# Kernel tuning notes

Measured on AMD Instinct MI355X. Metric: run time of the kernel, lower is better.

## Reference

```python
import jax, jax.numpy as jnp
import numpy as np

B, T, HID, NH = 2, 2048, 1024, 16
HD = HID // NH  # head_dim = 64
ROPE_BASE = 1000000.0


def _precompute_freqs(dim, end, rope_base):
    inv = 1.0 / (rope_base ** (np.arange(0, dim, 2)[: dim // 2].astype(np.float32) / dim))
    t = np.arange(end, dtype=np.float32)
    freqs = np.outer(t, inv).astype(np.float32)  # (end, dim//2)
    cos = np.concatenate([np.cos(freqs), np.cos(freqs)], axis=-1)
    sin = np.concatenate([np.sin(freqs), np.sin(freqs)], axis=-1)
    return jnp.asarray(cos), jnp.asarray(sin)


def setup_inputs() -> dict:
    key = jax.random.key(0)
    ks = jax.random.split(key, 5)
    x = jax.random.normal(ks[0], (B, T, HID), dtype=jnp.float32)
    s = 1.0 / np.sqrt(HID)
    Wq = jax.random.normal(ks[1], (HID, HID), dtype=jnp.float32) * s
    Wk = jax.random.normal(ks[2], (HID, HID), dtype=jnp.float32) * s
    Wv = jax.random.normal(ks[3], (HID, HID), dtype=jnp.float32) * s
    Wo = jax.random.normal(ks[4], (HID, HID), dtype=jnp.float32) * s
    cos, sin = _precompute_freqs(HD, T, ROPE_BASE)
    return {"x": x, "Wq": Wq, "Wk": Wk, "Wv": Wv, "Wo": Wo, "cos": cos, "sin": sin}


def _rotate_half(u):
    half = u.shape[-1] // 2
    return jnp.concatenate([-u[..., half:], u[..., :half]], axis=-1)


def reference(x, Wq, Wk, Wv, Wo, cos, sin):
    b, t, _ = x.shape
    # projections (nn.Linear: x @ W.T)
    q = (x @ Wq.T).reshape(b, t, NH, HD).transpose(0, 2, 1, 3)  # (B,H,T,D)
    k = (x @ Wk.T).reshape(b, t, NH, HD).transpose(0, 2, 1, 3)
    v = (x @ Wv.T).reshape(b, t, NH, HD).transpose(0, 2, 1, 3)
    c = cos[None, None, :t, :]
    s = sin[None, None, :t, :]
    q = q * c + _rotate_half(q) * s
    k = k * c + _rotate_half(k) * s
    scores = jnp.einsum("bhqd,bhkd->bhqk", q, k) / jnp.sqrt(jnp.float32(HD))
    causal = jnp.tril(jnp.ones((t, t), dtype=bool))
    scores = jnp.where(causal[None, None], scores, jnp.float32(-jnp.inf))
    prob = jax.nn.softmax(scores, axis=-1)
    out = jnp.einsum("bhqk,bhkd->bhqd", prob, v)
    out = out.transpose(0, 2, 1, 3).reshape(b, t, HID)
    return out @ Wo.T
```

## Files before the change

### kernel.cpp

```cpp
#include <hip/hip_runtime.h>
#include <hip/hip_bf16.h>

#define B_   2
#define T_   2048
#define HID_ 1024
#define NH_  16
#define HD_  64
#define K_   1024
#define M_   (B_*T_)

typedef __attribute__((ext_vector_type(8)))  short bf16x8;
typedef __attribute__((ext_vector_type(4)))  float f32x4;
typedef __attribute__((ext_vector_type(16))) float f32x16;
typedef __attribute__((ext_vector_type(4)))  unsigned int u32x4;
typedef __attribute__((ext_vector_type(2)))  unsigned int u32x2;

#define LOG2E 1.44269504088896340736f

__device__ inline unsigned short f2bf(float f) {
    __hip_bfloat16 h = __float2bfloat16(f);
    return __builtin_bit_cast(unsigned short, h);
}
__device__ inline unsigned int pk2(float a, float b) {
    return (unsigned int)f2bf(a) | ((unsigned int)f2bf(b) << 16);
}
__device__ inline unsigned int pkt(float a, float b) {
    return __builtin_amdgcn_perm(__builtin_bit_cast(unsigned, a),
                                 __builtin_bit_cast(unsigned, b), 0x03020706u);
}
__device__ inline bf16x8 cvt8(float4 a, float4 b) {
    bf16x8 r;
    r[0]=(short)f2bf(a.x); r[1]=(short)f2bf(a.y); r[2]=(short)f2bf(a.z); r[3]=(short)f2bf(a.w);
    r[4]=(short)f2bf(b.x); r[5]=(short)f2bf(b.y); r[6]=(short)f2bf(b.z); r[7]=(short)f2bf(b.w);
    return r;
}

__global__ __launch_bounds__(256)
void cast_all(const float* __restrict__ x,
              const float* __restrict__ W0, const float* __restrict__ W1,
              const float* __restrict__ W2, const float* __restrict__ W3,
              unsigned short* __restrict__ xo,
              unsigned short* __restrict__ o0, unsigned short* __restrict__ o1,
              unsigned short* __restrict__ o2, unsigned short* __restrict__ o3) {
    const int blk = blockIdx.x;
    const float* in;
    unsigned short* out;
    int i;
    if (blk < 2048) {
        in = x; out = xo; i = blk * 256 + threadIdx.x;
    } else {
        const int wb = blk - 2048, sec = wb >> 9;
        in  = (sec == 0) ? W0 : (sec == 1) ? W1 : (sec == 2) ? W2 : W3;
        out = (sec == 0) ? o0 : (sec == 1) ? o1 : (sec == 2) ? o2 : o3;
        i = (wb & 511) * 256 + threadIdx.x;
    }
    float4 a = ((const float4*)in)[2*i], b = ((const float4*)in)[2*i + 1];
    ((bf16x8*)out)[i] = cvt8(a, b);
}

template<int TYPE>
__global__ __launch_bounds__(256)
void gemm_k(const unsigned short* __restrict__ A, const unsigned short* __restrict__ W0,
            const unsigned short* __restrict__ W1, const unsigned short* __restrict__ W2,
            const float* __restrict__ cs, const float* __restrict__ sn,
            unsigned short* __restrict__ qb, unsigned short* __restrict__ kb,
            unsigned short* __restrict__ vtb, float* __restrict__ fout) {
    constexpr int BN = (TYPE == 1) ? 64 : 128;
    constexpr int NB = BN / 32;
    constexpr int NF = BN / 32;
    __shared__ unsigned short As[128*64];
    __shared__ unsigned short Bs[BN*64];
    const int tid = threadIdx.x;
    const int w = tid >> 6, lane = tid & 63;
    const int u = lane >> 4, c = lane & 15;
    const int bid = blockIdx.x;
    const int xcd = bid & 7, idx = bid >> 3;
    int bmi, bni;
    if constexpr (TYPE == 0) {
        bmi = (xcd & 3) * 8 + (idx & 7);
        bni = (xcd >> 2) * 12 + (idx >> 3);
    } else {
        bmi = (xcd & 3) * 8 + (idx & 7);
        bni = (xcd >> 2) * 8 + (idx >> 3);
    }
    const int bm = bmi * 128, bn = bni * BN;
    const int wm = (w & 1) * 64, wn = (w >> 1) * (BN / 2);
    const int srow = tid >> 3, scol = (tid & 7) << 3;

    const unsigned short* Wsec;
    int wrowbase;
    if constexpr (TYPE == 0) {
        const int sec = bn >> 10;
        Wsec = (sec == 0) ? W0 : ((sec == 1) ? W1 : W2);
        wrowbase = bn & 1023;
    } else {
        Wsec = W0;
        wrowbase = bn;
    }
    const unsigned short* Wp = Wsec + (size_t)(wrowbase + srow) * K_ + scol;
    const unsigned short* Ap = A + (size_t)(bm + srow) * K_ + scol;

    f32x4 acc[4][NF] = {};
    bf16x8 ra[4], rb[NB];

    auto loadin = [&](int k0) {
        #pragma unroll
        for (int i = 0; i < 4; ++i)
            ra[i] = *(const bf16x8*)(Ap + (size_t)i * 32 * K_ + k0);
        #pragma unroll
        for (int i = 0; i < NB; ++i)
            rb[i] = *(const bf16x8*)(Wp + (size_t)i * 32 * K_ + k0);
    };
    loadin(0);

    for (int k0 = 0; k0 < K_; k0 += 64) {
        __syncthreads();
        #pragma unroll
        for (int i = 0; i < 4; ++i) {
            const int row = i * 32 + srow;
            const int sc = (scol * 2) ^ ((row & 7) << 4);
            *(bf16x8*)((char*)As + row * 128 + sc) = ra[i];
        }
        #pragma unroll
        for (int i = 0; i < NB; ++i) {
            const int row = i * 32 + srow;
            const int sc = (scol * 2) ^ ((row & 7) << 4);
            *(bf16x8*)((char*)Bs + row * 128 + sc) = rb[i];
        }
        __syncthreads();
        if (k0 < K_ - 64) loadin(k0 + 64);
        #pragma unroll
        for (int kk = 0; kk < 2; ++kk) {
            bf16x8 af[4], bfr[NF];
            #pragma unroll
            for (int mi = 0; mi < 4; ++mi) {
                const int row = wm + mi * 16 + c;
                const int sc = (kk * 64 + u * 16) ^ ((row & 7) << 4);
                af[mi] = *(const bf16x8*)((char*)As + row * 128 + sc);
            }
            #pragma unroll
            for (int ni = 0; ni < NF; ++ni) {
                const int row = wn + ni * 16 + c;
                const int sc = (kk * 64 + u * 16) ^ ((row & 7) << 4);
                bfr[ni] = *(const bf16x8*)((char*)Bs + row * 128 + sc);
            }
            #pragma unroll
            for (int mi = 0; mi < 4; ++mi)
                #pragma unroll
                for (int ni = 0; ni < NF; ++ni)
                    acc[mi][ni] = __builtin_amdgcn_mfma_f32_16x16x32_bf16(
                        af[mi], bfr[ni], acc[mi][ni], 0, 0, 0);
        }
    }

    if constexpr (TYPE == 1) {
        #pragma unroll
        for (int mi = 0; mi < 4; ++mi)
            #pragma unroll
            for (int ni = 0; ni < NF; ++ni)
                #pragma unroll
                for (int r = 0; r < 4; ++r)
                    fout[(size_t)(bm + wm + 16*mi + 4*u + r) * HID_ + (bn + wn + 16*ni + c)] =
                        acc[mi][ni][r];
    } else {
        const int sec = bn >> 10;
        const int h = ((bn + wn) & 1023) >> 6;
        if (sec == 2) {
            #pragma unroll
            for (int mi = 0; mi < 4; ++mi)
                #pragma unroll
                for (int r = 0; r < 4; ++r) {
                    const int mg = bm + wm + 16*mi + 4*u + r;
                    const int bb = mg >> 11, t = mg & 2047;
                    const int tk = (t & ~12) | ((t & 4) << 1) | ((t & 8) >> 1);
                    #pragma unroll
                    for (int ni = 0; ni < 4; ++ni)
                        vtb[((size_t)(bb*16 + h) * 64 + 16*ni + c) * 2048 + tk] =
                            f2bf(acc[mi][ni][r]);
                }
        } else {
            unsigned short* ob = sec ? kb : qb;
            const float qsc = sec ? 1.0f : (0.125f * LOG2E);
            #pragma unroll
            for (int mi = 0; mi < 4; ++mi)
                #pragma unroll
                for (int r = 0; r < 4; ++r) {
                    const int mg = bm + wm + 16*mi + 4*u + r;
                    const int bb = mg >> 11, t = mg & 2047;
                    const size_t base = ((size_t)(bb*16 + h) * 2048 + t) * 64;
                    #pragma unroll
                    for (int ni = 0; ni < 2; ++ni) {
                        const int dlo = 16*ni + c;
                        const float cv = cs[t*64 + dlo], sv = sn[t*64 + dlo];
                        const float Aa = acc[mi][ni][r], Bb = acc[mi][ni+2][r];
                        ob[base + dlo]      = f2bf((Aa*cv - Bb*sv) * qsc);
                        ob[base + dlo + 32] = f2bf((Bb*cv + Aa*sv) * qsc);
                    }
                }
        }
    }
}

__global__ __launch_bounds__(256)
void attn18(const unsigned short* __restrict__ q, const unsigned short* __restrict__ k,
            const unsigned short* __restrict__ vt, unsigned short* __restrict__ ab) {
    const int raw = blockIdx.x;
    const int bh     = (raw & 7) + 8 * ((raw >> 3) & 3);
    const int qchunk = 15 - (raw >> 5);
    const int tid = threadIdx.x;
    const int wid = tid >> 6, lane = tid & 63;
    const int h = lane >> 5, c = lane & 31;
    const int b = bh >> 4, hh = bh & 15;
    const int q0 = qchunk * 128;
    const int qgcA = q0 + c, qgcB = q0 + 32 + c, qgcC = q0 + 64 + c, qgcD = q0 + 96 + c;
    const int stAd = 4 * qchunk;
    const int stBd = stAd + 1, stCd = stAd + 2, stDd = stAd + 3;
    const int NT   = stAd + 4;
    const unsigned short* qp = q  + (size_t)bh * (T_*64);
    const unsigned short* kp = k  + (size_t)bh * (T_*64);
    const unsigned short* vp = vt + (size_t)bh * (64*T_);

    const int kloff  = c * 64 + 8 * h;
    const int vloff0 = c * 2048 + 8 * h;
    const int vloff1 = vloff0 + 32 * 2048;

    bf16x8 qfA[4], qfB[4], qfC[4], qfD[4];
    {
        const unsigned short* qrowA = qp + (q0 + c) * 64 + 8 * h;
        #pragma unroll
        for (int s = 0; s < 4; ++s) {
            qfA[s] = *(const bf16x8*)(qrowA + s * 16);
            qfB[s] = *(const bf16x8*)(qrowA + 32 * 64 + s * 16);
            qfC[s] = *(const bf16x8*)(qrowA + 64 * 64 + s * 16);
            qfD[s] = *(const bf16x8*)(qrowA + 96 * 64 + s * 16);
        }
    }

    f32x16 OA0 = {}, OA1 = {}, OB0 = {}, OB1 = {};
    f32x16 OC0 = {}, OC1 = {}, OD0 = {}, OD1 = {};
    float mA = -1e30f, lA = 0.f, mB = -1e30f, lB = 0.f;
    float mC = -1e30f, lC = 0.f, mD = -1e30f, lD = 0.f;

    auto loadK = [&](bf16x8 (&kf)[4], int st) {
        const unsigned short* kst = kp + (st << 11);
        #pragma unroll
        for (int s = 0; s < 4; ++s)
            kf[s] = *(const bf16x8*)(kst + kloff + s * 16);
    };

    auto tileRest = [&](f32x16 sa, int st, int std_, int qgc,
                        float& m, float& l, f32x16& O0, f32x16& O1,
                        const bf16x8& vf0, const bf16x8& vf1,
                        const bf16x8& vf2, const bf16x8& vf3) {
        const int kvs = st << 5;
        float p[16];
        #pragma unroll
        for (int r = 0; r < 16; ++r) p[r] = sa[r];
        if (st == std_) {
            #pragma unroll
            for (int r = 0; r < 16; ++r) {
                const int kk = kvs + (r & 3) + 8 * (r >> 2) + 4 * h;
                if (kk > qgc) p[r] = -1e30f;
            }
        }
        const float a0 = fmaxf(fmaxf(p[0],  p[1]),  p[2]);
        const float a1 = fmaxf(fmaxf(p[3],  p[4]),  p[5]);
        const float a2 = fmaxf(fmaxf(p[6],  p[7]),  p[8]);
        const float a3 = fmaxf(fmaxf(p[9],  p[10]), p[11]);
        const float a4 = fmaxf(fmaxf(p[12], p[13]), p[14]);
        float mx = fmaxf(fmaxf(fmaxf(a0, a1), fmaxf(a2, a3)), fmaxf(a4, p[15]));
        if (!__all(mx <= m + 8.0f)) {
            mx = fmaxf(mx, __shfl_xor(mx, 32));
            const float mn = fmaxf(m, mx);
            const float f = __builtin_amdgcn_exp2f(m - mn);
            m = mn; l *= f;
            #pragma unroll
            for (int r = 0; r < 16; ++r) { O0[r] *= f; O1[r] *= f; }
        }
        float ps = 0.f;
        #pragma unroll
        for (int r = 0; r < 16; ++r) {
            p[r] = __builtin_amdgcn_exp2f(p[r] - m);
            ps += p[r];
        }
        l += ps;
        u32x4 B0w = { pkt(p[0],  p[1]),  pkt(p[2],  p[3]),
                      pkt(p[4],  p[5]),  pkt(p[6],  p[7])  };
        u32x4 B1w = { pkt(p[8],  p[9]),  pkt(p[10], p[11]),
                      pkt(p[12], p[13]), pkt(p[14], p[15]) };
        bf16x8 PB0 = __builtin_bit_cast(bf16x8, B0w);
        bf16x8 PB1 = __builtin_bit_cast(bf16x8, B1w);
        __builtin_amdgcn_s_setprio(1);
        O0 = __builtin_amdgcn_mfma_f32_32x32x16_bf16(vf0, PB0, O0, 0, 0, 0);
        O0 = __builtin_amdgcn_mfma_f32_32x32x16_bf16(vf1, PB1, O0, 0, 0, 0);
        O1 = __builtin_amdgcn_mfma_f32_32x32x16_bf16(vf2, PB0, O1, 0, 0, 0);
        O1 = __builtin_amdgcn_mfma_f32_32x32x16_bf16(vf3, PB1, O1, 0, 0, 0);
        __builtin_amdgcn_s_setprio(0);
    };

    auto qkt = [&](const bf16x8 (&kf)[4], const bf16x8 (&qf)[4]) -> f32x16 {
        __builtin_amdgcn_s_setprio(1);
        f32x16 sa = {};
        #pragma unroll
        for (int s = 0; s < 4; ++s)
            sa = __builtin_amdgcn_mfma_f32_32x32x16_bf16(kf[s], qf[s], sa, 0, 0, 0);
        __builtin_amdgcn_s_setprio(0);
        return sa;
    };

    bf16x8 kf_[4];
    if (wid < NT) {
        loadK(kf_, wid);
        for (int st = wid; st < NT; st += 4) {
            const unsigned short* vst = vp + (st << 5);
            bf16x8 vf0 = *(const bf16x8*)(vst + vloff0);
            bf16x8 vf1 = *(const bf16x8*)(vst + vloff0 + 16);
            bf16x8 vf2 = *(const bf16x8*)(vst + vloff1);
            bf16x8 vf3 = *(const bf16x8*)(vst + vloff1 + 16);
            const bool doA = (st <= stAd);
            const bool doB = (st <= stBd);
            const bool doC = (st <= stCd);
            if (doA) {
                f32x16 sa = qkt(kf_, qfA);
                tileRest(sa, st, stAd, qgcA, mA, lA, OA0, OA1, vf0, vf1, vf2, vf3);
            }
            if (doB) {
                f32x16 sa = qkt(kf_, qfB);
                tileRest(sa, st, stBd, qgcB, mB, lB, OB0, OB1, vf0, vf1, vf2, vf3);
            }
            if (doC) {
                f32x16 sa = qkt(kf_, qfC);
                tileRest(sa, st, stCd, qgcC, mC, lC, OC0, OC1, vf0, vf1, vf2, vf3);
            }
            {
                f32x16 sa = qkt(kf_, qfD);
                if (st + 4 < NT) loadK(kf_, st + 4);
                tileRest(sa, st, stDd, qgcD, mD, lD, OD0, OD1, vf0, vf1, vf2, vf3);
            }
        }
    }
    lA += __shfl_xor(lA, 32);
    lB += __shfl_xor(lB, 32);
    lC += __shfl_xor(lC, 32);
    lD += __shfl_xor(lD, 32);

    __shared__ unsigned OSu[4][128 * 34];
    __shared__ float mS[4][128], lS[4][128];
    if (h == 0) {
        mS[wid][c] = mA;      lS[wid][c] = lA;
        mS[wid][32 + c] = mB; lS[wid][32 + c] = lB;
        mS[wid][64 + c] = mC; lS[wid][64 + c] = lC;
        mS[wid][96 + c] = mD; lS[wid][96 + c] = lD;
    }
    {
        unsigned* os = &OSu[wid][0];
        const int rbA = c * 34 + 2 * h;
        const int rbB = (32 + c) * 34 + 2 * h;
        const int rbC = (64 + c) * 34 + 2 * h;
        const int rbD = (96 + c) * 34 + 2 * h;
        #pragma unroll
        for (int j = 0; j < 4; ++j) {
            os[rbA + 4*j]          = pk2(OA0[4*j],   OA0[4*j+1]);
            os[rbA + 4*j + 1]      = pk2(OA0[4*j+2], OA0[4*j+3]);
            os[rbA + 16 + 4*j]     = pk2(OA1[4*j],   OA1[4*j+1]);
            os[rbA + 16 + 4*j + 1] = pk2(OA1[4*j+2], OA1[4*j+3]);
            os[rbB + 4*j]          = pk2(OB0[4*j],   OB0[4*j+1]);
            os[rbB + 4*j + 1]      = pk2(OB0[4*j+2], OB0[4*j+3]);
            os[rbB + 16 + 4*j]     = pk2(OB1[4*j],   OB1[4*j+1]);
            os[rbB + 16 + 4*j + 1] = pk2(OB1[4*j+2], OB1[4*j+3]);
            os[rbC + 4*j]          = pk2(OC0[4*j],   OC0[4*j+1]);
            os[rbC + 4*j + 1]      = pk2(OC0[4*j+2], OC0[4*j+3]);
            os[rbC + 16 + 4*j]     = pk2(OC1[4*j],   OC1[4*j+1]);
            os[rbC + 16 + 4*j + 1] = pk2(OC1[4*j+2], OC1[4*j+3]);
            os[rbD + 4*j]          = pk2(OD0[4*j],   OD0[4*j+1]);
            os[rbD + 4*j + 1]      = pk2(OD0[4*j+2], OD0[4*j+3]);
            os[rbD + 16 + 4*j]     = pk2(OD1[4*j],   OD1[4*j+1]);
            os[rbD + 16 + 4*j + 1] = pk2(OD1[4*j+2], OD1[4*j+3]);
        }
    }
    __syncthreads();

    #pragma unroll
    for (int rr = 0; rr < 4; ++rr) {
        const int rl = rr * 32 + (tid & 31);
        const int ug = (tid >> 5) * 4;
        const float M = fmaxf(fmaxf(mS[0][rl], mS[1][rl]), fmaxf(mS[2][rl], mS[3][rl]));
        float acc[8] = {};
        float L = 0.f;
        #pragma unroll
        for (int w2 = 0; w2 < 4; ++w2) {
            const float sc = __builtin_amdgcn_exp2f(mS[w2][rl] - M);
            L += lS[w2][rl] * sc;
            u32x4 pa = *(u32x4*)&OSu[w2][rl * 34 + ug];
            #pragma unroll
            for (int t = 0; t < 4; ++t) {
                acc[2*t]   += __builtin_bit_cast(float, pa[t] << 16) * sc;
                acc[2*t+1] += __builtin_bit_cast(float, pa[t] & 0xffff0000u) * sc;
            }
        }
        const float inv = 1.0f / L;
        uint4 ov;
        ov.x = pk2(acc[0]*inv, acc[1]*inv);
        ov.y = pk2(acc[2]*inv, acc[3]*inv);
        ov.z = pk2(acc[4]*inv, acc[5]*inv);
        ov.w = pk2(acc[6]*inv, acc[7]*inv);
        *(uint4*)(ab + ((size_t)(b * T_) + q0 + rl) * HID_ + hh * 64 + ug * 2) = ov;
    }
}

extern "C" void kernel_launch(void* const* d_in, const int* in_sizes, int n_in,
                              void* d_out, int out_size, void* d_ws, size_t ws_size,
                              hipStream_t stream) {
    const float* x  = (const float*)d_in[0];
    const float* Wq = (const float*)d_in[1];
    const float* Wk = (const float*)d_in[2];
    const float* Wv = (const float*)d_in[3];
    const float* Wo = (const float*)d_in[4];
    const float* cs = (const float*)d_in[5];
    const float* sn = (const float*)d_in[6];
    char* wsb = (char*)d_ws;
    unsigned short* xb  = (unsigned short*)(wsb);
    unsigned short* wqb = (unsigned short*)(wsb + (8u  << 20));
    unsigned short* wkb = (unsigned short*)(wsb + (10u << 20));
    unsigned short* wvb = (unsigned short*)(wsb + (12u << 20));
    unsigned short* wob = (unsigned short*)(wsb + (14u << 20));
    unsigned short* qb  = (unsigned short*)(wsb + (16u << 20));
    unsigned short* kb  = (unsigned short*)(wsb + (24u << 20));
    unsigned short* vtb = (unsigned short*)(wsb + (32u << 20));
    unsigned short* ab  = (unsigned short*)(wsb + (40u << 20));

    cast_all<<<4096, 256, 0, stream>>>(x, Wq, Wk, Wv, Wo, xb, wqb, wkb, wvb, wob);

    gemm_k<0><<<768, 256, 0, stream>>>(
        xb, wqb, wkb, wvb, cs, sn, qb, kb, vtb, nullptr);
    attn18<<<512, 256, 0, stream>>>(qb, kb, vtb, ab);
    gemm_k<1><<<512, 256, 0, stream>>>(
        ab, wob, nullptr, nullptr, nullptr, nullptr,
        nullptr, nullptr, nullptr, (float*)d_out);
}
```

Baseline: 108.1 us.

## Use direct global-to-LDS loads with double-buffered shared tiles in GEMM

The projection GEMM now stages A and W tiles straight from global memory into LDS with global_load_lds, instead of going through registers. Two LDS buffers are used so the next K-slice can load while MFMAs run on the current one. This removes the register round-trip and one barrier per iteration. In exchange it doubles shared memory use, which may lower occupancy, and correctness relies on the swizzled per-lane addressing matching the existing read pattern and on the barrier covering the async LDS writes.

```diff
diff --git a/kernel.cpp b/kernel.cpp
--- a/kernel.cpp
+++ b/kernel.cpp
@@ -33,6 +33,11 @@
     r[0]=(short)f2bf(a.x); r[1]=(short)f2bf(a.y); r[2]=(short)f2bf(a.z); r[3]=(short)f2bf(a.w);
     r[4]=(short)f2bf(b.x); r[5]=(short)f2bf(b.y); r[6]=(short)f2bf(b.z); r[7]=(short)f2bf(b.w);
     return r;
+}
+__device__ inline void gll16(const void* g, void* l) {
+    __builtin_amdgcn_global_load_lds(
+        (const __attribute__((address_space(1))) unsigned int*)g,
+        (__attribute__((address_space(3))) unsigned int*)l, 16, 0, 0);
 }
 
 __global__ __launch_bounds__(256)
@@ -65,11 +70,11 @@
             const float* __restrict__ cs, const float* __restrict__ sn,
             unsigned short* __restrict__ qb, unsigned short* __restrict__ kb,
             unsigned short* __restrict__ vtb, float* __restrict__ fout) {
-    constexpr int BN = (TYPE == 1) ? 64 : 128;
-    constexpr int NB = BN / 32;
-    constexpr int NF = BN / 32;
-    __shared__ unsigned short As[128*64];
-    __shared__ unsigned short Bs[BN*64];
+    constexpr int BN    = (TYPE == 1) ? 64 : 128;
+    constexpr int NF    = BN / 32;
+    constexpr int NBSEG = BN / 32;
+    __shared__ unsigned short As[2][128*64];
+    __shared__ unsigned short Bs[2][BN*64];
     const int tid = threadIdx.x;
     const int w = tid >> 6, lane = tid & 63;
     const int u = lane >> 4, c = lane & 15;
@@ -85,7 +90,6 @@
     }
     const int bm = bmi * 128, bn = bni * BN;
     const int wm = (w & 1) * 64, wn = (w >> 1) * (BN / 2);
-    const int srow = tid >> 3, scol = (tid & 7) << 3;
 
     const unsigned short* Wsec;
     int wrowbase;
@@ -97,38 +101,33 @@
         Wsec = W0;
         wrowbase = bn;
     }
-    const unsigned short* Wp = Wsec + (size_t)(wrowbase + srow) * K_ + scol;
-    const unsigned short* Ap = A + (size_t)(bm + srow) * K_ + scol;
+    const unsigned short* Ab = A + (size_t)bm * K_;
+    const unsigned short* Wb = Wsec + (size_t)wrowbase * K_;
+    const int lrow8 = lane >> 3;
+    const int scolx = 8 * ((lane & 7) ^ (lrow8 & 7));
 
     f32x4 acc[4][NF] = {};
-    bf16x8 ra[4], rb[NB];
-
-    auto loadin = [&](int k0) {
-        #pragma unroll
-        for (int i = 0; i < 4; ++i)
-            ra[i] = *(const bf16x8*)(Ap + (size_t)i * 32 * K_ + k0);
-        #pragma unroll
-        for (int i = 0; i < NB; ++i)
-            rb[i] = *(const bf16x8*)(Wp + (size_t)i * 32 * K_ + k0);
+
+    auto stage = [&](int buf, int k0) {
+        #pragma unroll
+        for (int s4 = 0; s4 < 4; ++s4) {
+            const int seg = w * 4 + s4;
+            gll16(Ab + (size_t)(seg * 8 + lrow8) * K_ + k0 + scolx,
+                  (char*)&As[buf][0] + seg * 1024);
+        }
+        #pragma unroll
+        for (int s4 = 0; s4 < NBSEG; ++s4) {
+            const int seg = w * NBSEG + s4;
+            gll16(Wb + (size_t)(seg * 8 + lrow8) * K_ + k0 + scolx,
+                  (char*)&Bs[buf][0] + seg * 1024);
+        }
     };
-    loadin(0);
-
+
+    stage(0, 0);
+    __syncthreads();
+    int cur = 0;
     for (int k0 = 0; k0 < K_; k0 += 64) {
-        __syncthreads();
-        #pragma unroll
-        for (int i = 0; i < 4; ++i) {
-            const int row = i * 32 + srow;
-            const int sc = (scol * 2) ^ ((row & 7) << 4);
-            *(bf16x8*)((char*)As + row * 128 + sc) = ra[i];
-        }
-        #pragma unroll
-        for (int i = 0; i < NB; ++i) {
-            const int row = i * 32 + srow;
-            const int sc = (scol * 2) ^ ((row & 7) << 4);
-            *(bf16x8*)((char*)Bs + row * 128 + sc) = rb[i];
-        }
-        __syncthreads();
-        if (k0 < K_ - 64) loadin(k0 + 64);
+        if (k0 + 64 < K_) stage(cur ^ 1, k0 + 64);
         #pragma unroll
         for (int kk = 0; kk < 2; ++kk) {
             bf16x8 af[4], bfr[NF];
@@ -136,13 +135,13 @@
             for (int mi = 0; mi < 4; ++mi) {
                 const int row = wm + mi * 16 + c;
                 const int sc = (kk * 64 + u * 16) ^ ((row & 7) << 4);
-                af[mi] = *(const bf16x8*)((char*)As + row * 128 + sc);
+                af[mi] = *(const bf16x8*)((char*)&As[cur][0] + row * 128 + sc);
             }
             #pragma unroll
             for (int ni = 0; ni < NF; ++ni) {
                 const int row = wn + ni * 16 + c;
                 const int sc = (kk * 64 + u * 16) ^ ((row & 7) << 4);
-                bfr[ni] = *(const bf16x8*)((char*)Bs + row * 128 + sc);
+                bfr[ni] = *(const bf16x8*)((char*)&Bs[cur][0] + row * 128 + sc);
             }
             #pragma unroll
             for (int mi = 0; mi < 4; ++mi)
@@ -151,6 +150,8 @@
                     acc[mi][ni] = __builtin_amdgcn_mfma_f32_16x16x32_bf16(
                         af[mi], bfr[ni], acc[mi][ni], 0, 0, 0);
         }
+        __syncthreads();
+        cur ^= 1;
     }
 
     if constexpr (TYPE == 1) {
```

Measured after the change: 122.8 us. +13.6%, slower.
